# Optimization experiments

Measured on AMD Instinct MI355X. Metric: run time of the kernel, lower is better.

Reference implementation:

```python
import jax, jax.numpy as jnp
import numpy as np

U, T, K, Q, H = 4096, 200, 64, 10000, 128
STD_THETA = 1.0


def setup_inputs() -> dict:
    key = jax.random.key(0)
    ks = jax.random.split(key, 12)
    q_id = jax.random.randint(ks[0], (U, T), 0, Q, dtype=jnp.int32)
    resp = jax.random.randint(ks[1], (U, T), 0, 2, dtype=jnp.int32)
    # one KC per question so the per-timestep masked_select size is constant (= U)
    kc_of_q = jax.random.randint(ks[2], (Q,), 0, K)
    kmap = jax.nn.one_hot(kc_of_q, K, dtype=jnp.float32) > 0.5  # (Q, K) bool, one-hot
    mask = jnp.ones((U, T), dtype=bool)
    diff_mu = jax.random.normal(ks[3], (Q,), dtype=jnp.float32)
    disc_mu = jax.random.normal(ks[4], (Q,), dtype=jnp.float32)
    xav = lambda k, fi, fo: jax.random.normal(k, (fi, fo), dtype=jnp.float32) * (2.0 / (fi + fo)) ** 0.5
    W1 = xav(ks[5], 3, H)
    W2 = xav(ks[6], H, H)
    W3 = xav(ks[7], H, 2)
    b1 = jnp.zeros((H,), jnp.float32)
    b2 = jnp.zeros((H,), jnp.float32)
    b3 = jnp.zeros((2,), jnp.float32)
    return dict(mask=mask, q_id=q_id, kmap=kmap, resp=resp,
                diff_mu=diff_mu, disc_mu=disc_mu,
                W1=W1, b1=b1, W2=W2, b2=b2, W3=W3, b3=b3)


def reference(mask, q_id, kmap, resp, diff_mu, disc_mu, W1, b1, W2, b2, W3, b3):
    gelu = lambda x: jax.nn.gelu(x, approximate=False)  # torch nn.GELU default = exact erf
    nu = q_id.shape[0]
    td = diff_mu[q_id]                      # (U, T) trial difficulty
    ts = disc_mu[q_id]                      # (U, T) trial discrimination
    x = jnp.stack([td, ts, resp.astype(jnp.float32)], axis=-1)  # (U, T, 3)
    h = gelu(gelu(x @ W1 + b1) @ W2 + b2)
    out = gelu(h @ W3 + b3)                 # (U, T, 2)
    mu = out[..., 0].T                      # (T, U)
    logvar = out[..., 1].T                  # (T, U)
    std = jnp.maximum(jnp.exp(0.5 * logvar), 1e-8)
    r = (STD_THETA / std) ** 2              # (T, U)

    # backward Kalman-style recursion: b_t = 1/(1 + r_t + (1 - b_{t+1})), c_t = b_t*(c_{t+1} + r_t*mu_t)
    def bwd_step(carry, rm):
        b_n, c_n = carry
        r_t, mu_t = rm
        b_t = 1.0 / (1.0 + r_t + (1.0 - b_n))
        c_t = b_t * (c_n + r_t * mu_t)
        return (b_t, c_t), (b_t, c_t)

    init = (jnp.ones((nu,), mu.dtype), jnp.zeros((nu,), mu.dtype))
    _, (b_seq, c_seq) = jax.lax.scan(bwd_step, init, (r, mu), reverse=True)  # (T, U) each

    # forward pass: gather active-KC ability, update, scatter back into per-user KC state
    active_kc = jnp.argmax(kmap[q_id], axis=-1).T  # (T, U) one active KC per trial
    uidx = jnp.arange(nu)

    def fwd_step(curr, bck):
        b_t, c_t, kc_t = bck
        prev = curr[uidx, kc_t]
        mu_t = b_t * prev + c_t
        curr = curr.at[uidx, kc_t].set(mu_t)
        return curr, mu_t

    curr0 = jnp.zeros((nu, kmap.shape[1]), mu.dtype)
    last_ability_kc, ability_T = jax.lax.scan(fwd_step, curr0, (b_seq, c_seq, active_kc))
    ability = ability_T.T                   # (U, T): masked mean over one-hot KC = active KC ability
    trial_logits = ts * (ability - td)      # (U, T)
    return trial_logits, last_ability_kc
```

## Files before the change

kernel.cpp:

```cpp
#include <hip/hip_runtime.h>
#include <math.h>

#define U_ 4096
#define T_ 200
#define K_ 64
#define Q_ 10000
#define H_ 128
#define UPB 8
#define PPB 32

__device__ __forceinline__ float gelu_f(float x) {
  return 0.5f * x * (1.0f + erff(x * 0.70710678118654752440f));
}

__global__ __launch_bounds__(256, 4) void mlp_table_kernel(
    const float* __restrict__ diff_mu, const float* __restrict__ disc_mu,
    const float* __restrict__ W1, const float* __restrict__ b1,
    const float* __restrict__ W2, const float* __restrict__ b2,
    const float* __restrict__ W3, const float* __restrict__ b3,
    const unsigned char* __restrict__ kmap,
    float4* __restrict__ tab4, int* __restrict__ kc_of_q) {
  __shared__ float W2s[64 * H_];
  __shared__ float h1buf[PPB][H_ + 1];

  const int tid = threadIdx.x;
  const int lane = tid & 63, w = tid >> 6;
  const int base = blockIdx.x * PPB;

  if (blockIdx.x < 40) {
    int q = blockIdx.x * 256 + tid;
    if (q < Q_) {
      const unsigned char* km = kmap + (size_t)q * K_;
      int kc = 0;
#pragma unroll
      for (int k = 0; k < K_; ++k)
        if (km[k]) kc = k;
      kc_of_q[q] = kc;
    }
  }

  for (int v = tid; v < PPB * H_; v += 256) {
    int pl = v >> 7, j = v & 127;
    int pg = base + pl, q = pg >> 1;
    float rf = (float)(pg & 1);
    float a = fmaf(diff_mu[q], W1[j], b1[j]);
    a = fmaf(disc_mu[q], W1[H_ + j], a);
    a = fmaf(rf, W1[2 * H_ + j], a);
    h1buf[pl][j] = gelu_f(a);
  }
  for (int v = tid; v < 2048; v += 256)
    ((float4*)W2s)[v] = ((const float4*)W2)[v];
  __syncthreads();

  float a0[8], a1[8];
#pragma unroll
  for (int p = 0; p < 8; ++p) { a0[p] = 0.f; a1[p] = 0.f; }

#pragma clang loop unroll_count(4)
  for (int k = 0; k < 64; ++k) {
    float w0 = W2s[k * H_ + lane];
    float w1 = W2s[k * H_ + lane + 64];
#pragma unroll
    for (int p = 0; p < 8; ++p) {
      float hv = h1buf[w * 8 + p][k];
      a0[p] = fmaf(w0, hv, a0[p]);
      a1[p] = fmaf(w1, hv, a1[p]);
    }
  }
  __syncthreads();
  for (int v = tid; v < 2048; v += 256)
    ((float4*)W2s)[v] = ((const float4*)W2)[2048 + v];
  __syncthreads();
#pragma clang loop unroll_count(4)
  for (int k = 0; k < 64; ++k) {
    float w0 = W2s[k * H_ + lane];
    float w1 = W2s[k * H_ + lane + 64];
#pragma unroll
    for (int p = 0; p < 8; ++p) {
      float hv = h1buf[w * 8 + p][64 + k];
      a0[p] = fmaf(w0, hv, a0[p]);
      a1[p] = fmaf(w1, hv, a1[p]);
    }
  }

  float w30a = W3[lane * 2 + 0], w31a = W3[lane * 2 + 1];
  float w30b = W3[(lane + 64) * 2 + 0], w31b = W3[(lane + 64) * 2 + 1];
  float b2a = b2[lane], b2b = b2[lane + 64];
  float b30 = b3[0], b31 = b3[1];
#pragma unroll
  for (int p = 0; p < 8; ++p) {
    float h2a = gelu_f(a0[p] + b2a);
    float h2b = gelu_f(a1[p] + b2b);
    float s0 = h2a * w30a + h2b * w30b;
    float s1 = h2a * w31a + h2b * w31b;
#pragma unroll
    for (int off = 32; off > 0; off >>= 1) {
      s0 += __shfl_xor(s0, off, 64);
      s1 += __shfl_xor(s1, off, 64);
    }
    if (lane == 0) {
      float mu = gelu_f(s0 + b30);
      float lv = gelu_f(s1 + b31);
      float sd = fmaxf(expf(0.5f * lv), 1e-8f);
      int pg = base + w * 8 + p;
      int q = pg >> 1;
      tab4[pg] = make_float4(1.0f / (sd * sd), mu, disc_mu[q], diff_mu[q]);
    }
  }
}

__global__ __launch_bounds__(512) void scan_kernel(
    const int* __restrict__ q_id, const int* __restrict__ resp,
    const float4* __restrict__ tab4, const int* __restrict__ kc_of_q,
    float* __restrict__ out) {
  __shared__ float2 bcs[T_ * (UPB + 1)];
  __shared__ unsigned char kcs[T_ * UPB];

  const int tid = threadIdx.x;
  const int lane = tid & 63;
  const int ul = tid >> 6;
  const int gu = blockIdx.x * UPB + ul;

  float tts[4], ttd[4];
  const int* qrow = q_id + (size_t)gu * T_;
  const int* rrow = resp + (size_t)gu * T_;
#pragma unroll
  for (int i = 0; i < 4; ++i) {
    int t = i * 64 + lane;
    int tc = t < T_ ? t : T_ - 1;
    int q = qrow[tc];
    int rp = rrow[tc];
    float4 f = tab4[q * 2 + rp];
    tts[i] = f.z;
    ttd[i] = f.w;
    if (t < T_) {
      bcs[t * (UPB + 1) + ul] = make_float2(f.x, f.y);
      kcs[t * UPB + ul] = (unsigned char)kc_of_q[q];
    }
  }

  float tb[4], tcc[4];
  float b = 1.0f, c = 0.0f;
#pragma unroll 8
  for (int s = 7; s >= 0; --s) {
    int t = 192 + s;
    float2 rm = bcs[t * (UPB + 1) + ul];
    float x_ = 2.0f + rm.x - b;
    float ib = __builtin_amdgcn_rcpf(x_);
    ib = ib * (2.0f - x_ * ib);
    b = ib;
    c = b * fmaf(rm.x, rm.y, c);
    bool cap = (lane == s);
    tb[3] = cap ? b : tb[3];
    tcc[3] = cap ? c : tcc[3];
  }
#pragma unroll
  for (int i = 2; i >= 0; --i) {
#pragma unroll 8
    for (int s = 63; s >= 0; --s) {
      int t = i * 64 + s;
      float2 rm = bcs[t * (UPB + 1) + ul];
      float x_ = 2.0f + rm.x - b;
      float ib = __builtin_amdgcn_rcpf(x_);
      ib = ib * (2.0f - x_ * ib);
      b = ib;
      c = b * fmaf(rm.x, rm.y, c);
      bool cap = (lane == s);
      tb[i] = cap ? b : tb[i];
      tcc[i] = cap ? c : tcc[i];
    }
  }
#pragma unroll
  for (int i = 0; i < 4; ++i) {
    int t = i * 64 + lane;
    if (t < T_) bcs[t * (UPB + 1) + ul] = make_float2(tb[i], tcc[i]);
  }

  float x = 0.0f;
#pragma unroll 8
  for (int t = 0; t < T_; ++t) {
    float2 bc_ = bcs[t * (UPB + 1) + ul];
    int kc = (int)kcs[t * UPB + ul];
    float xn = fmaf(bc_.x, x, bc_.y);
    bool hit = (lane == kc);
    x = hit ? xn : x;
    if (hit) bcs[t * (UPB + 1) + ul].x = xn;
  }

  float* logits = out;
  float* last = out + (size_t)U_ * T_;
#pragma unroll
  for (int i = 0; i < 4; ++i) {
    int t = i * 64 + lane;
    if (t < T_) {
      float ab = bcs[t * (UPB + 1) + ul].x;
      logits[(size_t)gu * T_ + t] = tts[i] * (ab - ttd[i]);
    }
  }
  last[(size_t)gu * K_ + lane] = x;
}

extern "C" void kernel_launch(void* const* d_in, const int* in_sizes, int n_in,
                              void* d_out, int out_size, void* d_ws,
                              size_t ws_size, hipStream_t stream) {
  const int* q_id = (const int*)d_in[1];
  const unsigned char* kmap = (const unsigned char*)d_in[2];
  const int* resp = (const int*)d_in[3];
  const float* diff_mu = (const float*)d_in[4];
  const float* disc_mu = (const float*)d_in[5];
  const float* W1 = (const float*)d_in[6];
  const float* b1 = (const float*)d_in[7];
  const float* W2 = (const float*)d_in[8];
  const float* b2 = (const float*)d_in[9];
  const float* W3 = (const float*)d_in[10];
  const float* b3 = (const float*)d_in[11];
  float* out = (float*)d_out;
  char* ws = (char*)d_ws;

  auto align512 = [](size_t x) { return (x + 511) & ~(size_t)511; };
  size_t o = 0;
  float4* tab4 = (float4*)(ws + o);  o = align512(o + (size_t)2 * Q_ * 16);
  int* kc_of_q = (int*)(ws + o);     o = align512(o + (size_t)Q_ * 4);
  (void)ws_size; (void)in_sizes; (void)n_in; (void)out_size;

  mlp_table_kernel<<<Q_ * 2 / PPB, 256, 0, stream>>>(
      diff_mu, disc_mu, W1, b1, W2, b2, W3, b3, kmap, tab4, kc_of_q);
  scan_kernel<<<U_ / UPB, 512, 0, stream>>>(q_id, resp, tab4, kc_of_q, out);
}
```

Before: 138.8 us.

## Vectorize MLP shared-memory loads and emit logits directly from forward scan

The MLP kernel now reads W2 as float2 and h1 as float4 from LDS, which remaps output columns to adjacent pairs per lane and pads rows to 132 floats for alignment. It also loads b2 and W3 as vectors. The scan kernel stores the whole float4 table entry in LDS, so discrimination and difficulty no longer live in registers. The hitting lane then writes each logit straight to global memory inside the forward loop, removing the separate write-back pass. In exchange, LDS use in the scan kernel doubles, and the logit stores become scattered single-lane writes rather than coalesced ones.

Result: slower. 142.9 us (+3.0%).

```diff
diff --git a/kernel.cpp b/kernel.cpp
--- a/kernel.cpp
+++ b/kernel.cpp
@@ -20,8 +20,8 @@
     const float* __restrict__ W3, const float* __restrict__ b3,
     const unsigned char* __restrict__ kmap,
     float4* __restrict__ tab4, int* __restrict__ kc_of_q) {
-  __shared__ float W2s[64 * H_];
-  __shared__ float h1buf[PPB][H_ + 1];
+  __shared__ __align__(16) float W2s[64 * H_];
+  __shared__ __align__(16) float h1buf[PPB][H_ + 4];
 
   const int tid = threadIdx.x;
   const int lane = tid & 63, w = tid >> 6;
@@ -56,43 +56,50 @@
 #pragma unroll
   for (int p = 0; p < 8; ++p) { a0[p] = 0.f; a1[p] = 0.f; }
 
-#pragma clang loop unroll_count(4)
-  for (int k = 0; k < 64; ++k) {
-    float w0 = W2s[k * H_ + lane];
-    float w1 = W2s[k * H_ + lane + 64];
+#pragma clang loop unroll_count(2)
+  for (int kq = 0; kq < 64; kq += 4) {
+    float2 wv[4];
+#pragma unroll
+    for (int kk = 0; kk < 4; ++kk)
+      wv[kk] = *(const float2*)&W2s[(kq + kk) * H_ + 2 * lane];
 #pragma unroll
     for (int p = 0; p < 8; ++p) {
-      float hv = h1buf[w * 8 + p][k];
-      a0[p] = fmaf(w0, hv, a0[p]);
-      a1[p] = fmaf(w1, hv, a1[p]);
+      float4 hv = *(const float4*)&h1buf[w * 8 + p][kq];
+      a0[p] = fmaf(wv[0].x, hv.x, a0[p]); a1[p] = fmaf(wv[0].y, hv.x, a1[p]);
+      a0[p] = fmaf(wv[1].x, hv.y, a0[p]); a1[p] = fmaf(wv[1].y, hv.y, a1[p]);
+      a0[p] = fmaf(wv[2].x, hv.z, a0[p]); a1[p] = fmaf(wv[2].y, hv.z, a1[p]);
+      a0[p] = fmaf(wv[3].x, hv.w, a0[p]); a1[p] = fmaf(wv[3].y, hv.w, a1[p]);
     }
   }
   __syncthreads();
   for (int v = tid; v < 2048; v += 256)
     ((float4*)W2s)[v] = ((const float4*)W2)[2048 + v];
   __syncthreads();
-#pragma clang loop unroll_count(4)
-  for (int k = 0; k < 64; ++k) {
-    float w0 = W2s[k * H_ + lane];
-    float w1 = W2s[k * H_ + lane + 64];
+#pragma clang loop unroll_count(2)
+  for (int kq = 0; kq < 64; kq += 4) {
+    float2 wv[4];
+#pragma unroll
+    for (int kk = 0; kk < 4; ++kk)
+      wv[kk] = *(const float2*)&W2s[(kq + kk) * H_ + 2 * lane];
 #pragma unroll
     for (int p = 0; p < 8; ++p) {
-      float hv = h1buf[w * 8 + p][64 + k];
-      a0[p] = fmaf(w0, hv, a0[p]);
-      a1[p] = fmaf(w1, hv, a1[p]);
-    }
-  }
-
-  float w30a = W3[lane * 2 + 0], w31a = W3[lane * 2 + 1];
-  float w30b = W3[(lane + 64) * 2 + 0], w31b = W3[(lane + 64) * 2 + 1];
-  float b2a = b2[lane], b2b = b2[lane + 64];
+      float4 hv = *(const float4*)&h1buf[w * 8 + p][64 + kq];
+      a0[p] = fmaf(wv[0].x, hv.x, a0[p]); a1[p] = fmaf(wv[0].y, hv.x, a1[p]);
+      a0[p] = fmaf(wv[1].x, hv.y, a0[p]); a1[p] = fmaf(wv[1].y, hv.y, a1[p]);
+      a0[p] = fmaf(wv[2].x, hv.z, a0[p]); a1[p] = fmaf(wv[2].y, hv.z, a1[p]);
+      a0[p] = fmaf(wv[3].x, hv.w, a0[p]); a1[p] = fmaf(wv[3].y, hv.w, a1[p]);
+    }
+  }
+
+  float2 b2v = *(const float2*)&b2[2 * lane];
+  float4 w3v = *(const float4*)&W3[4 * lane];
   float b30 = b3[0], b31 = b3[1];
 #pragma unroll
   for (int p = 0; p < 8; ++p) {
-    float h2a = gelu_f(a0[p] + b2a);
-    float h2b = gelu_f(a1[p] + b2b);
-    float s0 = h2a * w30a + h2b * w30b;
-    float s1 = h2a * w31a + h2b * w31b;
+    float h2a = gelu_f(a0[p] + b2v.x);
+    float h2b = gelu_f(a1[p] + b2v.y);
+    float s0 = h2a * w3v.x + h2b * w3v.z;
+    float s1 = h2a * w3v.y + h2b * w3v.w;
 #pragma unroll
     for (int off = 32; off > 0; off >>= 1) {
       s0 += __shfl_xor(s0, off, 64);
@@ -113,7 +120,7 @@
     const int* __restrict__ q_id, const int* __restrict__ resp,
     const float4* __restrict__ tab4, const int* __restrict__ kc_of_q,
     float* __restrict__ out) {
-  __shared__ float2 bcs[T_ * (UPB + 1)];
+  __shared__ __align__(16) float4 q4s[T_ * (UPB + 1)];
   __shared__ unsigned char kcs[T_ * UPB];
 
   const int tid = threadIdx.x;
@@ -121,20 +128,15 @@
   const int ul = tid >> 6;
   const int gu = blockIdx.x * UPB + ul;
 
-  float tts[4], ttd[4];
   const int* qrow = q_id + (size_t)gu * T_;
   const int* rrow = resp + (size_t)gu * T_;
 #pragma unroll
   for (int i = 0; i < 4; ++i) {
     int t = i * 64 + lane;
-    int tc = t < T_ ? t : T_ - 1;
-    int q = qrow[tc];
-    int rp = rrow[tc];
-    float4 f = tab4[q * 2 + rp];
-    tts[i] = f.z;
-    ttd[i] = f.w;
     if (t < T_) {
-      bcs[t * (UPB + 1) + ul] = make_float2(f.x, f.y);
+      int q = qrow[t];
+      int rp = rrow[t];
+      q4s[t * (UPB + 1) + ul] = tab4[q * 2 + rp];
       kcs[t * UPB + ul] = (unsigned char)kc_of_q[q];
     }
   }
@@ -144,7 +146,7 @@
 #pragma unroll 8
   for (int s = 7; s >= 0; --s) {
     int t = 192 + s;
-    float2 rm = bcs[t * (UPB + 1) + ul];
+    float2 rm = *(const float2*)&q4s[t * (UPB + 1) + ul];
     float x_ = 2.0f + rm.x - b;
     float ib = __builtin_amdgcn_rcpf(x_);
     ib = ib * (2.0f - x_ * ib);
@@ -159,7 +161,7 @@
 #pragma unroll 8
     for (int s = 63; s >= 0; --s) {
       int t = i * 64 + s;
-      float2 rm = bcs[t * (UPB + 1) + ul];
+      float2 rm = *(const float2*)&q4s[t * (UPB + 1) + ul];
       float x_ = 2.0f + rm.x - b;
       float ib = __builtin_amdgcn_rcpf(x_);
       ib = ib * (2.0f - x_ * ib);
@@ -173,29 +175,21 @@
 #pragma unroll
   for (int i = 0; i < 4; ++i) {
     int t = i * 64 + lane;
-    if (t < T_) bcs[t * (UPB + 1) + ul] = make_float2(tb[i], tcc[i]);
+    if (t < T_)
+      *(float2*)&q4s[t * (UPB + 1) + ul] = make_float2(tb[i], tcc[i]);
   }
 
   float x = 0.0f;
+  float* logits = out + (size_t)gu * T_;
+  float* last = out + (size_t)U_ * T_;
 #pragma unroll 8
   for (int t = 0; t < T_; ++t) {
-    float2 bc_ = bcs[t * (UPB + 1) + ul];
+    float4 g = q4s[t * (UPB + 1) + ul];
     int kc = (int)kcs[t * UPB + ul];
-    float xn = fmaf(bc_.x, x, bc_.y);
+    float xn = fmaf(g.x, x, g.y);
     bool hit = (lane == kc);
     x = hit ? xn : x;
-    if (hit) bcs[t * (UPB + 1) + ul].x = xn;
-  }
-
-  float* logits = out;
-  float* last = out + (size_t)U_ * T_;
-#pragma unroll
-  for (int i = 0; i < 4; ++i) {
-    int t = i * 64 + lane;
-    if (t < T_) {
-      float ab = bcs[t * (UPB + 1) + ul].x;
-      logits[(size_t)gu * T_ + t] = tts[i] * (ab - ttd[i]);
-    }
+    if (hit) logits[t] = g.z * (xn - g.w);
   }
   last[(size_t)gu * K_ + lane] = x;
 }
```
